# Performance work log

Measured on AMD Instinct MI355X. Metric: run time of the kernel, lower is better.

## Reference

```python
import jax, jax.numpy as jnp
import numpy as np

FEAT_DIM = 128

def conv3(x, w, b):
    y = jax.lax.conv_general_dilated(x, w, (1, 1), 'SAME', dimension_numbers=('NCHW', 'OIHW', 'NCHW'))
    return y + b[None, :, None, None]

def edsr(x, hw, hb, rw, rb, tw, tb):
    # EDSR baseline encoder (no upsampling): head conv, n resblocks, tail conv, global skip
    x = conv3(x, hw, hb)
    res = x
    for i in range(rw.shape[0]):
        t = jax.nn.relu(conv3(res, rw[i, 0], rb[i, 0]))
        res = res + conv3(t, rw[i, 1], rb[i, 1])
    return conv3(res, tw, tb) + x

def maxpool(x, k):
    return jax.lax.reduce_window(x, -jnp.inf, jax.lax.max, (1, 1, k, k), (1, 1, k, k), 'VALID')

def make_coord(h, w):
    ys = -1.0 + (2.0 * jnp.arange(h, dtype=jnp.float32) + 1.0) / h
    xs = -1.0 + (2.0 * jnp.arange(w, dtype=jnp.float32) + 1.0) / w
    yy, xx = jnp.meshgrid(ys, xs, indexing='ij')
    return jnp.stack([yy, xx], axis=-1)  # [h,w,2] (y,x)

def sample_nearest(img, coord):
    # F.grid_sample nearest, align_corners=False, zeros padding.
    # img [b,c,hi,wi]; coord [b,N,2] normalized (y,x) -> [b,N,c]
    b, c, hi, wi = img.shape
    iy = jnp.round(((coord[..., 0] + 1.0) * hi - 1.0) / 2.0)
    ix = jnp.round(((coord[..., 1] + 1.0) * wi - 1.0) / 2.0)
    valid = (iy >= 0) & (iy < hi) & (ix >= 0) & (ix < wi)
    idx = (jnp.clip(iy, 0, hi - 1) * wi + jnp.clip(ix, 0, wi - 1)).astype(jnp.int32)
    out = jnp.take_along_axis(img.reshape(b, c, hi * wi), idx[:, None, :], axis=2)
    out = jnp.where(valid[:, None, :], out, jnp.zeros((), img.dtype))
    return out.transpose(0, 2, 1)

def mlp2(x, w1, b1, w2, b2):
    return jax.nn.gelu(x @ w1 + b1, approximate=False) @ w2 + b2

def level(feat, coord, hr_guide, hr_guide_lr, im_w, im_b, wg, ffn, residual):
    b, c, h, w = feat.shape
    Hh, Ww = hr_guide.shape[2], hr_guide.shape[3]
    N = coord.shape[0]
    coord = jnp.broadcast_to(coord[None], (b, N, 2))
    fc = jnp.broadcast_to(make_coord(h, w).transpose(2, 0, 1)[None], (b, 2, h, w))
    g_s = sample_nearest(hr_guide, coord)  # [b,N,guide_dim]
    scale = jnp.array([h, w], dtype=jnp.float32)
    preds = []
    for vx in (-1.0, 1.0):
        for vy in (-1.0, 1.0):
            coord_ = coord + jnp.array([vx / h, vy / w], dtype=jnp.float32)
            f_s = sample_nearest(feat, coord_)
            gl_s = sample_nearest(hr_guide_lr, coord_)
            c_s = sample_nearest(fc, coord_)
            rel = (coord - c_s) * scale
            inp = jnp.concatenate([f_s, g_s, gl_s, rel], axis=-1)  # [b,N,3*fd+2]
            pred = jax.nn.relu(inp @ im_w + im_b)  # MLP(hidden_list=None): Linear+ReLU
            preds.append(pred[..., :FEAT_DIM])
            preds.append(pred[..., FEAT_DIM:])
    preds = jnp.stack(preds, axis=-2)  # [b,N,8,fd]
    weight = jax.nn.softmax(mlp2(preds, *wg), axis=-2)
    recon = jnp.sum(preds * weight, axis=-2)  # [b,N,fd]
    out = mlp2(recon, *ffn)
    if residual:
        out = out + recon
    return out.transpose(0, 2, 1).reshape(b, -1, Hh, Ww)

def setup_inputs():
    ks = jax.random.split(jax.random.key(0), 24)
    fd, nb, nsb = 128, 31, 3
    B, H, W, hlr = 16, 64, 64, 16
    def w_(k, shape, fan):
        return jax.random.normal(k, shape, dtype=jnp.float32) * (fan ** -0.5)
    return {
        'HR_MSI': jax.random.normal(ks[0], (B, nsb, H, W), dtype=jnp.float32),
        'lms': jax.random.normal(ks[1], (B, nb, H, W), dtype=jnp.float32),
        'LR_HSI': jax.random.normal(ks[2], (B, nb, hlr, hlr), dtype=jnp.float32),
        'spa_head_w': w_(ks[3], (fd, nsb + nb, 3, 3), (nsb + nb) * 9), 'spa_head_b': jnp.zeros((fd,)),
        'spa_res_w': w_(ks[4], (4, 2, fd, fd, 3, 3), fd * 9), 'spa_res_b': jnp.zeros((4, 2, fd)),
        'spa_tail_w': w_(ks[5], (fd, fd, 3, 3), fd * 9), 'spa_tail_b': jnp.zeros((fd,)),
        'spe_head_w': w_(ks[6], (fd, nb, 3, 3), nb * 9), 'spe_head_b': jnp.zeros((fd,)),
        'spe_res_w': w_(ks[7], (4, 2, fd, fd, 3, 3), fd * 9), 'spe_res_b': jnp.zeros((4, 2, fd)),
        'spe_tail_w': w_(ks[8], (fd, fd, 3, 3), fd * 9), 'spe_tail_b': jnp.zeros((fd,)),
        'l1_w': w_(ks[9], (fd * 3 + 2, fd * 2), fd * 3 + 2), 'l1_b': jnp.zeros((fd * 2,)),
        'wg32_w1': w_(ks[10], (fd, 64), fd), 'wg32_b1': jnp.zeros((64,)),
        'wg32_w2': w_(ks[11], (64, fd), 64), 'wg32_b2': jnp.zeros((fd,)),
        'ffn32_w1': w_(ks[12], (fd, 64), fd), 'ffn32_b1': jnp.zeros((64,)),
        'ffn32_w2': w_(ks[13], (64, fd), 64), 'ffn32_b2': jnp.zeros((fd,)),
        'l2_w': w_(ks[14], (fd * 3 + 2, fd * 2), fd * 3 + 2), 'l2_b': jnp.zeros((fd * 2,)),
        'wg64_w1': w_(ks[15], (fd, 64), fd), 'wg64_b1': jnp.zeros((64,)),
        'wg64_w2': w_(ks[16], (64, fd), 64), 'wg64_b2': jnp.zeros((fd,)),
        'ffn64_w1': w_(ks[17], (fd, 64), fd), 'ffn64_b1': jnp.zeros((64,)),
        'ffn64_w2': w_(ks[18], (64, nb), 64), 'ffn64_b2': jnp.zeros((nb,)),
    }

def reference(HR_MSI, lms, LR_HSI, spa_head_w, spa_head_b, spa_res_w, spa_res_b, spa_tail_w, spa_tail_b, spe_head_w, spe_head_b, spe_res_w, spe_res_b, spe_tail_w, spe_tail_b, l1_w, l1_b, wg32_w1, wg32_b1, wg32_w2, wg32_b2, ffn32_w1, ffn32_b1, ffn32_w2, ffn32_b2, l2_w, l2_b, wg64_w1, wg64_b1, wg64_w2, wg64_b2, ffn64_w1, ffn64_b1, ffn64_w2, ffn64_b2):
    b, _, H, W = HR_MSI.shape
    hr_spa = edsr(jnp.concatenate([HR_MSI, lms], axis=1), spa_head_w, spa_head_b, spa_res_w, spa_res_b, spa_tail_w, spa_tail_b)
    guide32 = maxpool(hr_spa, H // 32)   # AdaptiveMaxPool2d -> 32x32
    guide16 = maxpool(hr_spa, H // 16)   # AdaptiveMaxPool2d -> 16x16
    lr_spe = edsr(LR_HSI, spe_head_w, spe_head_b, spe_res_w, spe_res_b, spe_tail_w, spe_tail_b)
    coord32 = make_coord(H // 2, W // 2).reshape(-1, 2)
    coord64 = make_coord(H, W).reshape(-1, 2)
    l1 = level(lr_spe, coord32, guide32, guide16, l1_w, l1_b, (wg32_w1, wg32_b1, wg32_w2, wg32_b2), (ffn32_w1, ffn32_b1, ffn32_w2, ffn32_b2), True)
    l2 = level(l1, coord64, hr_spa, guide32, l2_w, l2_b, (wg64_w1, wg64_b1, wg64_w2, wg64_b2), (ffn64_w1, ffn64_b1, ffn64_w2, ffn64_b2), False)
    return lms + l2
```

## Files before the change

kernel.cpp:

```cpp
#include <hip/hip_runtime.h>
#include <math.h>

typedef _Float16 f16;
typedef __attribute__((ext_vector_type(4))) _Float16 f16x4;
typedef __attribute__((ext_vector_type(8))) _Float16 f16x8;
typedef __attribute__((ext_vector_type(4))) float f32x4;
typedef __attribute__((ext_vector_type(4))) unsigned int u32x4;

__device__ __forceinline__ float gelu_f(float x) {
    float xs = x * 0.70710678118654752440f;
    float ax = fabsf(xs);
    float t = __builtin_amdgcn_rcpf(1.0f + 0.3275911f * ax);
    float p = t * (0.254829592f + t * (-0.284496736f + t * (1.421413741f +
              t * (-1.453152027f + t * 1.061405429f))));
    float erfv = 1.0f - p * __expf(-ax * ax);
    erfv = copysignf(erfv, xs);
    return 0.5f * x * (1.0f + erfv);
}

__device__ __forceinline__ void nsamp(float cy, float cx, int hi, int wi,
                                      int& iy, int& ix, bool& valid) {
    float fy = rintf(((cy + 1.0f) * (float)hi - 1.0f) * 0.5f);
    float fx = rintf(((cx + 1.0f) * (float)wi - 1.0f) * 0.5f);
    valid = (fy >= 0.0f) && (fy < (float)hi) && (fx >= 0.0f) && (fx < (float)wi);
    iy = (int)fminf(fmaxf(fy, 0.0f), (float)(hi - 1));
    ix = (int)fminf(fmaxf(fx, 0.0f), (float)(wi - 1));
}

__global__ __launch_bounds__(256) void pack_w(
    const float* __restrict__ src, f16* __restrict__ dst,
    int Cin, int NCHUNK, int total) {
    int i = blockIdx.x * 256 + threadIdx.x;
    if (i >= total) return;
    int ci = i & 31;
    int tap = (i >> 5) % 9;
    int q = i / 288;
    int chunk = q % NCHUNK;
    int q2 = q / NCHUNK;
    int cout = q2 & 127;
    int conv = q2 >> 7;
    int cin = chunk * 32 + ci;
    float v = (cin < Cin) ? src[((size_t)(conv * 128 + cout) * Cin + cin) * 9 + tap] : 0.f;
    dst[i] = (f16)v;
}

__global__ __launch_bounds__(256) void pack_lvl(
    const float* __restrict__ src, f16* __restrict__ dst,
    int Ksrc, int N, int NC) {
    int i = blockIdx.x * 256 + threadIdx.x;
    if (i >= N * NC * 32) return;
    int kk = i & 31;
    int c = (i >> 5) % NC;
    int n = i / (32 * NC);
    int k = c * 32 + kk;
    dst[i] = (f16)((k < Ksrc) ? src[(size_t)k * N + n] : 0.f);
}

__global__ __launch_bounds__(256) void build_cc(
    const float* __restrict__ msi, const float* __restrict__ lms,
    f16* __restrict__ out, int total) {
    int i = blockIdx.x * 256 + threadIdx.x;
    if (i >= total) return;
    int ch = i % 34;
    int p = i / 34;
    int x = p & 63, y = (p >> 6) & 63, b = p >> 12;
    float v = (ch < 3) ? msi[(((size_t)(b * 3 + ch) << 6) + y << 6) + x]
                       : lms[(((size_t)(b * 31 + ch - 3) << 6) + y << 6) + x];
    out[((size_t)(b * 66 + y + 1) * 66 + x + 1) * 64 + ch] = v;
}

__global__ __launch_bounds__(256) void build_spe(
    const float* __restrict__ in, f16* __restrict__ out, int total) {
    int i = blockIdx.x * 256 + threadIdx.x;
    if (i >= total) return;
    int ch = i % 31;
    int p = i / 31;
    int x = p & 15, y = (p >> 4) & 15, b = p >> 8;
    out[((size_t)(b * 18 + y + 1) * 18 + x + 1) * 32 + ch] =
        (f16)in[(((size_t)(b * 31 + ch) << 4) + y << 4) + x];
}

template<int PXW, int XSH, int ROWS, int WAVES, int NCHUNK>
__global__ __launch_bounds__(WAVES * 64, 4) void conv_mfma(
    const f16* __restrict__ in_h,
    const f16* __restrict__ wp, const float* __restrict__ bias,
    const f16* __restrict__ skip_h, f16* __restrict__ out_h,
    f16* __restrict__ out2, int mode) {
    constexpr int XW = 1 << XSH;
    constexpr int PH = XW + 2;
    constexpr int NPX = (ROWS + 2) * PXW;
    constexpr int UPP = NCHUNK * 4;
    constexpr int UNITS = NPX * UPP;
    constexpr int NTH = WAVES * 64;
    constexpr int ITER = (UNITS + NTH - 1) / NTH;
    constexpr int WN = WAVES / 2;
    constexpr int NT = 8 / WN;
    constexpr int MT = (ROWS << XSH) >> 5;
    constexpr int PXB = NCHUNK * 64;
    __shared__ char ldsb[NPX * PXB];

    int tid = threadIdx.x;
    constexpr int NYB = XW / ROWS;
    int b = blockIdx.x / NYB;
    int y0 = (blockIdx.x % NYB) * ROWS;
    int wave = tid >> 6, lane = tid & 63;
    int wm = wave / WN, wn = wave % WN;
    int l15 = lane & 15, lk = lane >> 4;

#pragma unroll
    for (int i = 0; i < ITER; ++i) {
        int u = tid + NTH * i;
        if (u < UNITS) {
            int px = u / UPP, kg = u % UPP;
            int r = px / PXW, xp = px - r * PXW;
            u32x4 v = *(const u32x4*)(in_h +
                (size_t)((b * PH + y0 + r) * PXW + xp) * (NCHUNK * 32) + kg * 8);
            *(u32x4*)(ldsb + ((u * 16) ^ ((px & 7) << 4))) = v;
        }
    }
    __syncthreads();

    f32x4 acc[MT][NT];
#pragma unroll
    for (int mt = 0; mt < MT; ++mt)
#pragma unroll
        for (int nt = 0; nt < NT; ++nt)
            acc[mt][nt] = (f32x4){0.f, 0.f, 0.f, 0.f};

#pragma unroll
    for (int c = 0; c < NCHUNK; ++c) {
#pragma unroll
        for (int tap = 0; tap < 9; ++tap) {
            const int dy = tap / 3, dx = tap % 3;
            f16x8 afr[MT];
#pragma unroll
            for (int mt = 0; mt < MT; ++mt) {
                int px = (wm * MT + mt) * 16 + l15;
                int row = px >> XSH, x = px & (XW - 1);
                int pxl = (row + dy) * PXW + x + dx;
                int la = pxl * PXB + c * 64 + lk * 16;
                afr[mt] = *(const f16x8*)(ldsb + (la ^ ((pxl & 7) << 4)));
            }
#pragma unroll
            for (int nt = 0; nt < NT; ++nt) {
                int cout = wn * (NT * 16) + nt * 16 + l15;
                f16x8 bfr = *(const f16x8*)(wp + ((size_t)(cout * NCHUNK + c) * 9 + tap) * 32 + lk * 8);
#pragma unroll
                for (int mt = 0; mt < MT; ++mt)
                    acc[mt][nt] = __builtin_amdgcn_mfma_f32_16x16x32_f16(afr[mt], bfr, acc[mt][nt], 0, 0, 0);
            }
        }
    }

#pragma unroll
    for (int mt = 0; mt < MT; ++mt)
#pragma unroll
        for (int nt = 0; nt < NT; ++nt) {
            int cout = wn * (NT * 16) + nt * 16 + l15;
            float bv = bias[cout];
#pragma unroll
            for (int reg = 0; reg < 4; ++reg) {
                int px = (wm * MT + mt) * 16 + lk * 4 + reg;
                int row = px >> XSH, x = px & (XW - 1);
                int yim = y0 + row;
                float vv = acc[mt][nt][reg] + bv;
                size_t ah = ((size_t)(b * PH + yim + 1) * PXW + x + 1) * 128 + cout;
                if (mode == 1) vv = fmaxf(vv, 0.f);
                if (mode == 2) vv += (float)out_h[ah];
                if (mode == 3) {
                    vv += (float)skip_h[ah];
                    out2[((size_t)((b << XSH) + yim) << XSH | x) * 128 + cout] = (f16)vv;
                } else if (mode == 4) {
                    f16 hv = (f16)vv;
                    out_h[ah] = hv;
                    out2[ah] = hv;
                } else {
                    out_h[ah] = (f16)vv;
                }
            }
        }
}

__global__ __launch_bounds__(256) void maxpool_nhwc(
    const f16* __restrict__ in, f16* __restrict__ out,
    int H, int W, int k, int total) {
    int i = blockIdx.x * 256 + threadIdx.x;
    if (i >= total) return;
    int c = i & 127;
    int r = i >> 7;
    int Wo = W / k, Ho = H / k;
    int x = r % Wo; r /= Wo;
    int y = r % Ho;
    int b = r / Ho;
    float m = -3.402823466e38f;
    for (int dy = 0; dy < k; ++dy)
        for (int dx = 0; dx < k; ++dx)
            m = fmaxf(m, (float)in[((size_t)(b * H + y * k + dy) * W + x * k + dx) * 128 + c]);
    out[i] = (f16)m;
}

__global__ __launch_bounds__(256) void level_kernel(
    const f16* __restrict__ featT, int fh, int fw,
    const f16* __restrict__ guideT, int Hg, int Wg,
    const f16* __restrict__ glrT, int hl, int wl,
    int Hq, int Wq, int n_per_b,
    const f16* __restrict__ imw_h, const float* __restrict__ imb,
    const f16* __restrict__ w1h, const float* __restrict__ b1,
    const f16* __restrict__ w2h, const float* __restrict__ b2,
    const f16* __restrict__ f1h, const float* __restrict__ fb1,
    const f16* __restrict__ f2h, const float* __restrict__ fb2,
    int odim, int residual, int out_nchw,
    const float* __restrict__ lms,
    f16* __restrict__ out16, float* __restrict__ outf) {
    __shared__ char smem[58624];
    f16* s_inp  = (f16*)smem;
    f16* s_pred = (f16*)smem;
    f16* s_h1   = (f16*)(smem + 34816);
    f16* s_hh   = (f16*)smem;
    f16* s_rec  = (f16*)(smem + 54272);

    int tid = threadIdx.x;
    int b = blockIdx.x / n_per_b;
    int n0 = (blockIdx.x % n_per_b) * 16;
    float invHq = 1.0f / (float)Hq, invWq = 1.0f / (float)Wq;
    float invfh = 1.0f / (float)fh, invfw = 1.0f / (float)fw;
    int wave = tid >> 6, lane = tid & 63;
    int l15 = lane & 15, lk = lane >> 4;

    {
        const int r64 = tid >> 2, t4 = tid & 3;
        const int cidx = r64 >> 4, q = r64 & 15;
        int n = n0 + q;
        int qy = n / Wq, qx = n - qy * Wq;
        float cy = -1.0f + (float)(2 * qy + 1) * invHq;
        float cx = -1.0f + (float)(2 * qx + 1) * invWq;
        float vxc = (cidx < 2) ? -1.0f : 1.0f;
        float vyc = (cidx & 1) ? 1.0f : -1.0f;
        float cy_ = cy + vxc * invfh;
        float cx_ = cx + vyc * invfw;
        int iy, ix; bool vf;
        nsamp(cy_, cx_, fh, fw, iy, ix, vf);
        const f16* fp = featT + ((size_t)(b * fh + iy) * fw + ix) * 128;
        int gy, gx; bool vg0;
        nsamp(cy, cx, Hg, Wg, gy, gx, vg0);
        const f16* gp = guideT + ((size_t)(b * Hg + gy) * Wg + gx) * 128;
        int ly, lx; bool vl;
        nsamp(cy_, cx_, hl, wl, ly, lx, vl);
        const f16* lp = glrT + ((size_t)(b * hl + ly) * wl + lx) * 128;
        f16* row = s_inp + r64 * 424;
        const u32x4 zz = (u32x4){0, 0, 0, 0};
#pragma unroll
        for (int e = 0; e < 4; ++e) {
            int d0 = t4 * 8 + e * 32;
            u32x4 av = vf ? *(const u32x4*)(fp + d0) : zz;
            u32x4 gv = vg0 ? *(const u32x4*)(gp + d0) : zz;
            u32x4 lv = vl ? *(const u32x4*)(lp + d0) : zz;
            *(u32x4*)(row + d0) = av;
            *(u32x4*)(row + 128 + d0) = gv;
            *(u32x4*)(row + 256 + d0) = lv;
        }
        if (t4 == 0) {
#pragma unroll
            for (int e = 0; e < 4; ++e)
                *(u32x4*)((char*)row + 768 + e * 16) = zz;
            float csy = vf ? (-1.0f + (float)(2 * iy + 1) * invfh) : 0.0f;
            float csx = vf ? (-1.0f + (float)(2 * ix + 1) * invfw) : 0.0f;
            row[384] = (f16)((cy - csy) * (float)fh);
            row[385] = (f16)((cx - csx) * (float)fw);
        }
    }
    __syncthreads();

    f32x4 acc[4][4];
    {
#pragma unroll
        for (int mt = 0; mt < 4; ++mt)
#pragma unroll
            for (int nt = 0; nt < 4; ++nt)
                acc[mt][nt] = (f32x4){0.f, 0.f, 0.f, 0.f};
        int nbase = wave * 64;
#pragma unroll
        for (int ks = 0; ks < 13; ++ks) {
            f16x8 afr[4];
#pragma unroll
            for (int mt = 0; mt < 4; ++mt)
                afr[mt] = *(const f16x8*)((char*)s_inp + (mt * 16 + l15) * 848 + ks * 64 + lk * 16);
#pragma unroll
            for (int nt = 0; nt < 4; ++nt) {
                f16x8 bfr = *(const f16x8*)(imw_h + ((size_t)(nbase + nt * 16 + l15) * 13 + ks) * 32 + lk * 8);
#pragma unroll
                for (int mt = 0; mt < 4; ++mt)
                    acc[mt][nt] = __builtin_amdgcn_mfma_f32_16x16x32_f16(afr[mt], bfr, acc[mt][nt], 0, 0, 0);
            }
        }
    }
    __syncthreads();

    {
        int nbase = wave * 64;
#pragma unroll
        for (int nt = 0; nt < 4; ++nt) {
            int col = nbase + nt * 16 + l15;
            float bv = imb[col];
            int j_hi = col >> 7, d = col & 127;
#pragma unroll
            for (int mt = 0; mt < 4; ++mt)
#pragma unroll
                for (int reg = 0; reg < 4; ++reg) {
                    int row64 = mt * 16 + lk * 4 + reg;
                    int q = row64 & 15, cidx = row64 >> 4;
                    int qj = q * 8 + cidx * 2 + j_hi;
                    s_pred[qj * 136 + d] = (f16)fmaxf(acc[mt][nt][reg] + bv, 0.f);
                }
        }
    }
    __syncthreads();

    {
        f32x4 a1[8];
#pragma unroll
        for (int mt = 0; mt < 8; ++mt) a1[mt] = (f32x4){0.f, 0.f, 0.f, 0.f};
        int c1 = wave * 16 + l15;
#pragma unroll
        for (int ks = 0; ks < 4; ++ks) {
            f16x8 bfr = *(const f16x8*)(w1h + ((size_t)c1 * 4 + ks) * 32 + lk * 8);
#pragma unroll
            for (int mt = 0; mt < 8; ++mt) {
                f16x8 afr = *(const f16x8*)((char*)s_pred + (mt * 16 + l15) * 272 + ks * 64 + lk * 16);
                a1[mt] = __builtin_amdgcn_mfma_f32_16x16x32_f16(afr, bfr, a1[mt], 0, 0, 0);
            }
        }
        float bb1 = b1[c1];
#pragma unroll
        for (int mt = 0; mt < 8; ++mt)
#pragma unroll
            for (int reg = 0; reg < 4; ++reg) {
                int row = mt * 16 + lk * 4 + reg;
                s_h1[row * 72 + c1] = (f16)gelu_f(a1[mt][reg] + bb1);
            }
    }
    __syncthreads();

    {
        f32x4 a2[8][2];
#pragma unroll
        for (int mt = 0; mt < 8; ++mt) {
            a2[mt][0] = (f32x4){0.f, 0.f, 0.f, 0.f};
            a2[mt][1] = (f32x4){0.f, 0.f, 0.f, 0.f};
        }
#pragma unroll
        for (int ks = 0; ks < 2; ++ks) {
#pragma unroll
            for (int nt = 0; nt < 2; ++nt) {
                int c2 = wave * 32 + nt * 16 + l15;
                f16x8 bfr = *(const f16x8*)(w2h + ((size_t)c2 * 2 + ks) * 32 + lk * 8);
#pragma unroll
                for (int mt = 0; mt < 8; ++mt) {
                    f16x8 afr = *(const f16x8*)((char*)s_h1 + (mt * 16 + l15) * 144 + ks * 64 + lk * 16);
                    a2[mt][nt] = __builtin_amdgcn_mfma_f32_16x16x32_f16(afr, bfr, a2[mt][nt], 0, 0, 0);
                }
            }
        }
        int qhalf = lk >> 1;
#pragma unroll
        for (int nt = 0; nt < 2; ++nt) {
            int col = wave * 32 + nt * 16 + l15;
            float bb2 = b2[col];
#pragma unroll
            for (int mt = 0; mt < 8; ++mt) {
                int q = mt * 2 + qhalf;
                float v[4];
                float mloc = -3.4e38f;
#pragma unroll
                for (int reg = 0; reg < 4; ++reg) {
                    v[reg] = a2[mt][nt][reg] + bb2;
                    mloc = fmaxf(mloc, v[reg]);
                }
                float mf = fmaxf(mloc, __shfl_xor(mloc, 16));
                float e[4], sl = 0.f;
#pragma unroll
                for (int reg = 0; reg < 4; ++reg) {
                    e[reg] = __expf(v[reg] - mf);
                    sl += e[reg];
                }
                float sf = sl + __shfl_xor(sl, 16);
                float inv = 1.0f / sf;
                float rp = 0.f;
#pragma unroll
                for (int reg = 0; reg < 4; ++reg) {
                    int row = mt * 16 + lk * 4 + reg;
                    rp += (float)s_pred[row * 136 + col] * e[reg];
                }
                rp *= inv;
                float rf = rp + __shfl_xor(rp, 16);
                if ((lk & 1) == 0) s_rec[q * 136 + col] = (f16)rf;
            }
        }
    }
    __syncthreads();

    {
        f32x4 a1 = (f32x4){0.f, 0.f, 0.f, 0.f};
        int c1 = wave * 16 + l15;
#pragma unroll
        for (int ks = 0; ks < 4; ++ks) {
            f16x8 afr = *(const f16x8*)((char*)s_rec + l15 * 272 + ks * 64 + lk * 16);
            f16x8 bfr = *(const f16x8*)(f1h + ((size_t)c1 * 4 + ks) * 32 + lk * 8);
            a1 = __builtin_amdgcn_mfma_f32_16x16x32_f16(afr, bfr, a1, 0, 0, 0);
        }
        float bb = fb1[c1];
#pragma unroll
        for (int reg = 0; reg < 4; ++reg) {
            int row = lk * 4 + reg;
            s_hh[row * 72 + c1] = (f16)gelu_f(a1[reg] + bb);
        }
    }
    __syncthreads();

    if (!out_nchw) {
        f32x4 a2[2];
        a2[0] = (f32x4){0.f, 0.f, 0.f, 0.f};
        a2[1] = (f32x4){0.f, 0.f, 0.f, 0.f};
#pragma unroll
        for (int ks = 0; ks < 2; ++ks) {
            f16x8 afr = *(const f16x8*)((char*)s_hh + l15 * 144 + ks * 64 + lk * 16);
#pragma unroll
            for (int nt = 0; nt < 2; ++nt) {
                int col = wave * 32 + nt * 16 + l15;
                f16x8 bfr = *(const f16x8*)(f2h + ((size_t)col * 2 + ks) * 32 + lk * 8);
                a2[nt] = __builtin_amdgcn_mfma_f32_16x16x32_f16(afr, bfr, a2[nt], 0, 0, 0);
            }
        }
#pragma unroll
        for (int nt = 0; nt < 2; ++nt) {
            int col = wave * 32 + nt * 16 + l15;
            float bb = fb2[col];
#pragma unroll
            for (int reg = 0; reg < 4; ++reg) {
                int q = lk * 4 + reg;
                int n = n0 + q;
                int qy = n / Wq, qx = n - qy * Wq;
                float val = a2[nt][reg] + bb;
                if (residual) val += (float)s_rec[q * 136 + col];
                out16[((size_t)(b * Hq + qy) * Wq + qx) * 128 + col] = (f16)val;
            }
        }
    } else {
        if (wave < 2) {
            f32x4 a2 = (f32x4){0.f, 0.f, 0.f, 0.f};
#pragma unroll
            for (int ks = 0; ks < 2; ++ks) {
                f16x8 afr = *(const f16x8*)((char*)s_hh + l15 * 144 + ks * 64 + lk * 16);
                int col = wave * 16 + l15;
                f16x8 bfr = *(const f16x8*)(f2h + ((size_t)col * 2 + ks) * 32 + lk * 8);
                a2 = __builtin_amdgcn_mfma_f32_16x16x32_f16(afr, bfr, a2, 0, 0, 0);
            }
            int d = wave * 16 + l15;
            if (d < odim) {
                float bb = fb2[d];
#pragma unroll
                for (int reg = 0; reg < 4; ++reg) {
                    int q = lk * 4 + reg;
                    int n = n0 + q;
                    int qy = n / Wq, qx = n - qy * Wq;
                    size_t oi = (((size_t)b * odim + d) * Hq + qy) * Wq + qx;
                    outf[oi] = a2[reg] + bb + lms[oi];
                }
            }
        }
    }
}

#define WPACK_B   0ull
#define CC_B      5529600ull
#define SPEIN_B   (CC_B)
#define X2_B      (CC_B + 331776ull)
#define R2_B      (CC_B + 1658880ull)
#define T2_B      (CC_B + 2985984ull)
#define RH_B      14450688ull
#define TH_B      32292864ull
#define XH_B      50135040ull
#define G32_B     (TH_B)
#define G16_B     (TH_B + 4194304ull)
#define L1T_B     (TH_B + 5242880ull)
#define LRSPE_B   (CC_B + 4313088ull)
#define HR16_B    67977216ull
#define LVLW_B    101531648ull
#define L1IMW_B   (LVLW_B)
#define L1W1_B    (LVLW_B + 212992ull)
#define L1W2_B    (LVLW_B + 229376ull)
#define L1F1_B    (LVLW_B + 245760ull)
#define L1F2_B    (LVLW_B + 262144ull)
#define L2IMW_B   (LVLW_B + 278528ull)
#define L2W1_B    (LVLW_B + 491520ull)
#define L2W2_B    (LVLW_B + 507904ull)
#define L2F1_B    (LVLW_B + 524288ull)
#define L2F2_B    (LVLW_B + 540672ull)

extern "C" void kernel_launch(void* const* d_in, const int* in_sizes, int n_in,
                              void* d_out, int out_size, void* d_ws, size_t ws_size,
                              hipStream_t stream) {
    (void)in_sizes; (void)n_in; (void)out_size; (void)ws_size;
    const float* HR_MSI     = (const float*)d_in[0];
    const float* lms        = (const float*)d_in[1];
    const float* LR_HSI     = (const float*)d_in[2];
    const float* spa_head_w = (const float*)d_in[3];
    const float* spa_head_b = (const float*)d_in[4];
    const float* spa_res_w  = (const float*)d_in[5];
    const float* spa_res_b  = (const float*)d_in[6];
    const float* spa_tail_w = (const float*)d_in[7];
    const float* spa_tail_b = (const float*)d_in[8];
    const float* spe_head_w = (const float*)d_in[9];
    const float* spe_head_b = (const float*)d_in[10];
    const float* spe_res_w  = (const float*)d_in[11];
    const float* spe_res_b  = (const float*)d_in[12];
    const float* spe_tail_w = (const float*)d_in[13];
    const float* spe_tail_b = (const float*)d_in[14];
    const float* l1_w   = (const float*)d_in[15];
    const float* l1_b   = (const float*)d_in[16];
    const float* wg32_w1 = (const float*)d_in[17];
    const float* wg32_b1 = (const float*)d_in[18];
    const float* wg32_w2 = (const float*)d_in[19];
    const float* wg32_b2 = (const float*)d_in[20];
    const float* ffn32_w1 = (const float*)d_in[21];
    const float* ffn32_b1 = (const float*)d_in[22];
    const float* ffn32_w2 = (const float*)d_in[23];
    const float* ffn32_b2 = (const float*)d_in[24];
    const float* l2_w   = (const float*)d_in[25];
    const float* l2_b   = (const float*)d_in[26];
    const float* wg64_w1 = (const float*)d_in[27];
    const float* wg64_b1 = (const float*)d_in[28];
    const float* wg64_w2 = (const float*)d_in[29];
    const float* wg64_b2 = (const float*)d_in[30];
    const float* ffn64_w1 = (const float*)d_in[31];
    const float* ffn64_b1 = (const float*)d_in[32];
    const float* ffn64_w2 = (const float*)d_in[33];
    const float* ffn64_b2 = (const float*)d_in[34];

    char* ws = (char*)d_ws;
    f16* Wp      = (f16*)(ws + WPACK_B);
    f16* Cc      = (f16*)(ws + CC_B);
    f16* SPEin   = (f16*)(ws + SPEIN_B);
    f16* X2h     = (f16*)(ws + X2_B);
    f16* R2h     = (f16*)(ws + R2_B);
    f16* T2h     = (f16*)(ws + T2_B);
    f16* lrspe16 = (f16*)(ws + LRSPE_B);
    f16* Rh      = (f16*)(ws + RH_B);
    f16* Xh      = (f16*)(ws + XH_B);
    f16* Th      = (f16*)(ws + TH_B);
    f16* g32T    = (f16*)(ws + G32_B);
    f16* g16T    = (f16*)(ws + G16_B);
    f16* l1T16   = (f16*)(ws + L1T_B);
    f16* hr16    = (f16*)(ws + HR16_B);
    f16* l1imw = (f16*)(ws + L1IMW_B);
    f16* l1w1  = (f16*)(ws + L1W1_B);
    f16* l1w2  = (f16*)(ws + L1W2_B);
    f16* l1f1  = (f16*)(ws + L1F1_B);
    f16* l1f2  = (f16*)(ws + L1F2_B);
    f16* l2imw = (f16*)(ws + L2IMW_B);
    f16* l2w1  = (f16*)(ws + L2W1_B);
    f16* l2w2  = (f16*)(ws + L2W2_B);
    f16* l2f1  = (f16*)(ws + L2F1_B);
    f16* l2f2  = (f16*)(ws + L2F2_B);

    hipMemsetAsync(ws + CC_B, 0, 8921088ull, stream);
    hipMemsetAsync(ws + RH_B, 0, 53526528ull, stream);

    pack_w<<<288, 256, 0, stream>>>(spa_head_w, Wp + 0, 34, 2, 73728);
    pack_w<<<4608, 256, 0, stream>>>(spa_res_w, Wp + 73728, 128, 4, 1179648);
    pack_w<<<576, 256, 0, stream>>>(spa_tail_w, Wp + 1253376, 128, 4, 147456);
    pack_w<<<144, 256, 0, stream>>>(spe_head_w, Wp + 1400832, 31, 1, 36864);
    pack_w<<<4608, 256, 0, stream>>>(spe_res_w, Wp + 1437696, 128, 4, 1179648);
    pack_w<<<576, 256, 0, stream>>>(spe_tail_w, Wp + 2617344, 128, 4, 147456);

    pack_lvl<<<416, 256, 0, stream>>>(l1_w, l1imw, 386, 256, 13);
    pack_lvl<<<32, 256, 0, stream>>>(wg32_w1, l1w1, 128, 64, 4);
    pack_lvl<<<32, 256, 0, stream>>>(wg32_w2, l1w2, 64, 128, 2);
    pack_lvl<<<32, 256, 0, stream>>>(ffn32_w1, l1f1, 128, 64, 4);
    pack_lvl<<<32, 256, 0, stream>>>(ffn32_w2, l1f2, 64, 128, 2);
    pack_lvl<<<416, 256, 0, stream>>>(l2_w, l2imw, 386, 256, 13);
    pack_lvl<<<32, 256, 0, stream>>>(wg64_w1, l2w1, 128, 64, 4);
    pack_lvl<<<32, 256, 0, stream>>>(wg64_w2, l2w2, 64, 128, 2);
    pack_lvl<<<32, 256, 0, stream>>>(ffn64_w1, l2f1, 128, 64, 4);
    pack_lvl<<<8, 256, 0, stream>>>(ffn64_w2, l2f2, 64, 31, 2);

    build_cc<<<8704, 256, 0, stream>>>(HR_MSI, lms, Cc, 16 * 64 * 64 * 34);
    conv_mfma<66, 6, 2, 8, 2><<<512, 512, 0, stream>>>(Cc, Wp + 0, spa_head_b,
                                                       nullptr, Xh, Rh, 4);
    hipMemsetAsync(ws + SPEIN_B, 0, 5361664ull, stream);
    for (int i = 0; i < 4; ++i) {
        conv_mfma<66, 6, 2, 8, 4><<<512, 512, 0, stream>>>(
            Rh, Wp + 73728 + (size_t)(2 * i) * 147456, spa_res_b + 2 * i * 128,
            nullptr, Th, nullptr, 1);
        conv_mfma<66, 6, 2, 8, 4><<<512, 512, 0, stream>>>(
            Th, Wp + 73728 + (size_t)(2 * i + 1) * 147456, spa_res_b + (2 * i + 1) * 128,
            nullptr, Rh, nullptr, 2);
    }
    conv_mfma<66, 6, 2, 8, 4><<<512, 512, 0, stream>>>(Rh, Wp + 1253376, spa_tail_b,
                                                       Xh, nullptr, hr16, 3);

    maxpool_nhwc<<<8192, 256, 0, stream>>>(hr16, g32T, 64, 64, 2, 2097152);
    maxpool_nhwc<<<2048, 256, 0, stream>>>(hr16, g16T, 64, 64, 4, 524288);

    build_spe<<<496, 256, 0, stream>>>(LR_HSI, SPEin, 16 * 16 * 16 * 31);
    conv_mfma<18, 4, 2, 4, 1><<<128, 256, 0, stream>>>(SPEin, Wp + 1400832, spe_head_b,
                                                       nullptr, X2h, R2h, 4);
    for (int i = 0; i < 4; ++i) {
        conv_mfma<18, 4, 2, 4, 4><<<128, 256, 0, stream>>>(
            R2h, Wp + 1437696 + (size_t)(2 * i) * 147456, spe_res_b + 2 * i * 128,
            nullptr, T2h, nullptr, 1);
        conv_mfma<18, 4, 2, 4, 4><<<128, 256, 0, stream>>>(
            T2h, Wp + 1437696 + (size_t)(2 * i + 1) * 147456, spe_res_b + (2 * i + 1) * 128,
            nullptr, R2h, nullptr, 2);
    }
    conv_mfma<18, 4, 2, 4, 4><<<128, 256, 0, stream>>>(R2h, Wp + 2617344, spe_tail_b,
                                                       X2h, nullptr, lrspe16, 3);

    level_kernel<<<1024, 256, 0, stream>>>(
        lrspe16, 16, 16, g32T, 32, 32, g16T, 16, 16,
        32, 32, 64,
        l1imw, l1_b, l1w1, wg32_b1, l1w2, wg32_b2,
        l1f1, ffn32_b1, l1f2, ffn32_b2,
        128, 1, 0, nullptr, l1T16, nullptr);

    level_kernel<<<4096, 256, 0, stream>>>(
        l1T16, 32, 32, hr16, 64, 64, g32T, 32, 32,
        64, 64, 256,
        l2imw, l2_b, l2w1, wg64_b1, l2w2, wg64_b2,
        l2f1, ffn64_b1, l2f2, ffn64_b2,
        31, 0, 1, lms, nullptr, (float*)d_out);
}
```

Before: 1.027 ms.

## Co-schedule spatial and spectral EDSR convs in shared launches, merge maxpools

Adds a dual-conv kernel that dispatches blocks to either the high-resolution spatial EDSR conv or the low-resolution spectral EDSR conv based on block index. The two independent encoders now run in the same launches, so the small spectral convs fill the machine alongside the large ones instead of running serially. The spectral buffers get their own workspace region so they no longer alias buffers still in use, and the two maxpools become one launch. The spectral path now runs with 8 waves instead of 4, which may change its tiling efficiency.

Measured after the change: 941.7 us. 1.09x faster.

```diff
diff --git a/kernel.cpp b/kernel.cpp
--- a/kernel.cpp
+++ b/kernel.cpp
@@ -81,7 +81,8 @@
 }
 
 template<int PXW, int XSH, int ROWS, int WAVES, int NCHUNK>
-__global__ __launch_bounds__(WAVES * 64, 4) void conv_mfma(
+__device__ __forceinline__ void conv_body(
+    int bx, char* ldsb,
     const f16* __restrict__ in_h,
     const f16* __restrict__ wp, const float* __restrict__ bias,
     const f16* __restrict__ skip_h, f16* __restrict__ out_h,
@@ -97,12 +98,11 @@
     constexpr int NT = 8 / WN;
     constexpr int MT = (ROWS << XSH) >> 5;
     constexpr int PXB = NCHUNK * 64;
-    __shared__ char ldsb[NPX * PXB];
 
     int tid = threadIdx.x;
     constexpr int NYB = XW / ROWS;
-    int b = blockIdx.x / NYB;
-    int y0 = (blockIdx.x % NYB) * ROWS;
+    int b = bx / NYB;
+    int y0 = (bx % NYB) * ROWS;
     int wave = tid >> 6, lane = tid & 63;
     int wm = wave / WN, wn = wave % WN;
     int l15 = lane & 15, lk = lane >> 4;
@@ -181,22 +181,57 @@
         }
 }
 
-__global__ __launch_bounds__(256) void maxpool_nhwc(
-    const f16* __restrict__ in, f16* __restrict__ out,
-    int H, int W, int k, int total) {
+template<int PXW1, int XSH1, int ROWS1, int NCH1,
+         int PXW2, int XSH2, int ROWS2, int NCH2, int WAVES>
+__global__ __launch_bounds__(WAVES * 64, 4) void conv_dual(
+    int g1,
+    const f16* __restrict__ in1, const f16* __restrict__ wp1,
+    const float* __restrict__ bi1, const f16* __restrict__ sk1,
+    f16* __restrict__ o1h, f16* __restrict__ o1b,
+    const f16* __restrict__ in2, const f16* __restrict__ wp2,
+    const float* __restrict__ bi2, const f16* __restrict__ sk2,
+    f16* __restrict__ o2h, f16* __restrict__ o2b,
+    int mode) {
+    constexpr int B1 = (ROWS1 + 2) * PXW1 * NCH1 * 64;
+    constexpr int B2 = (ROWS2 + 2) * PXW2 * NCH2 * 64;
+    constexpr int MAXB = B1 > B2 ? B1 : B2;
+    __shared__ char ldsb[MAXB];
+    int bx = blockIdx.x;
+    if (bx < g1)
+        conv_body<PXW1, XSH1, ROWS1, WAVES, NCH1>(bx, ldsb, in1, wp1, bi1, sk1, o1h, o1b, mode);
+    else
+        conv_body<PXW2, XSH2, ROWS2, WAVES, NCH2>(bx - g1, ldsb, in2, wp2, bi2, sk2, o2h, o2b, mode);
+}
+
+__global__ __launch_bounds__(256) void maxpool_both(
+    const f16* __restrict__ in, f16* __restrict__ o2, f16* __restrict__ o4) {
     int i = blockIdx.x * 256 + threadIdx.x;
-    if (i >= total) return;
-    int c = i & 127;
-    int r = i >> 7;
-    int Wo = W / k, Ho = H / k;
-    int x = r % Wo; r /= Wo;
-    int y = r % Ho;
-    int b = r / Ho;
-    float m = -3.402823466e38f;
-    for (int dy = 0; dy < k; ++dy)
-        for (int dx = 0; dx < k; ++dx)
-            m = fmaxf(m, (float)in[((size_t)(b * H + y * k + dy) * W + x * k + dx) * 128 + c]);
-    out[i] = (f16)m;
+    if (i < 2097152) {
+        int c = i & 127;
+        int r = i >> 7;
+        int x = r & 31; r >>= 5;
+        int y = r & 31; r >>= 5;
+        int b = r;
+        float m = -3.402823466e38f;
+        for (int dy = 0; dy < 2; ++dy)
+            for (int dx = 0; dx < 2; ++dx)
+                m = fmaxf(m, (float)in[((size_t)((b * 64 + y * 2 + dy)) * 64 + x * 2 + dx) * 128 + c]);
+        o2[i] = (f16)m;
+    } else {
+        int j = i - 2097152;
+        if (j < 524288) {
+            int c = j & 127;
+            int r = j >> 7;
+            int x = r & 15; r >>= 4;
+            int y = r & 15; r >>= 4;
+            int b = r;
+            float m = -3.402823466e38f;
+            for (int dy = 0; dy < 4; ++dy)
+                for (int dx = 0; dx < 4; ++dx)
+                    m = fmaxf(m, (float)in[((size_t)((b * 64 + y * 4 + dy)) * 64 + x * 4 + dx) * 128 + c]);
+            o4[j] = (f16)m;
+        }
+    }
 }
 
 __global__ __launch_bounds__(256) void level_kernel(
@@ -473,17 +508,12 @@
 
 #define WPACK_B   0ull
 #define CC_B      5529600ull
-#define SPEIN_B   (CC_B)
-#define X2_B      (CC_B + 331776ull)
-#define R2_B      (CC_B + 1658880ull)
-#define T2_B      (CC_B + 2985984ull)
 #define RH_B      14450688ull
 #define TH_B      32292864ull
 #define XH_B      50135040ull
 #define G32_B     (TH_B)
 #define G16_B     (TH_B + 4194304ull)
 #define L1T_B     (TH_B + 5242880ull)
-#define LRSPE_B   (CC_B + 4313088ull)
 #define HR16_B    67977216ull
 #define LVLW_B    101531648ull
 #define L1IMW_B   (LVLW_B)
@@ -496,6 +526,12 @@
 #define L2W2_B    (LVLW_B + 507904ull)
 #define L2F1_B    (LVLW_B + 524288ull)
 #define L2F2_B    (LVLW_B + 540672ull)
+#define SPE2_B    102088704ull
+#define SPEIN_B   (SPE2_B)
+#define X2_B      (SPE2_B + 331776ull)
+#define R2_B      (SPE2_B + 1658880ull)
+#define T2_B      (SPE2_B + 2985984ull)
+#define LRSPE_B   (SPE2_B + 4313088ull)
 
 extern "C" void kernel_launch(void* const* d_in, const int* in_sizes, int n_in,
                               void* d_out, int out_size, void* d_ws, size_t ws_size,
@@ -565,6 +601,7 @@
 
     hipMemsetAsync(ws + CC_B, 0, 8921088ull, stream);
     hipMemsetAsync(ws + RH_B, 0, 53526528ull, stream);
+    hipMemsetAsync(ws + SPE2_B, 0, 5361664ull, stream);
 
     pack_w<<<288, 256, 0, stream>>>(spa_head_w, Wp + 0, 34, 2, 73728);
     pack_w<<<4608, 256, 0, stream>>>(spa_res_w, Wp + 73728, 128, 4, 1179648);
@@ -585,36 +622,28 @@
     pack_lvl<<<8, 256, 0, stream>>>(ffn64_w2, l2f2, 64, 31, 2);
 
     build_cc<<<8704, 256, 0, stream>>>(HR_MSI, lms, Cc, 16 * 64 * 64 * 34);
-    conv_mfma<66, 6, 2, 8, 2><<<512, 512, 0, stream>>>(Cc, Wp + 0, spa_head_b,
-                                                       nullptr, Xh, Rh, 4);
-    hipMemsetAsync(ws + SPEIN_B, 0, 5361664ull, stream);
+    build_spe<<<496, 256, 0, stream>>>(LR_HSI, SPEin, 16 * 16 * 16 * 31);
+
+    conv_dual<66, 6, 2, 2, 18, 4, 2, 1, 8><<<640, 512, 0, stream>>>(
+        512,
+        Cc, Wp + 0, spa_head_b, nullptr, Xh, Rh,
+        SPEin, Wp + 1400832, spe_head_b, nullptr, X2h, R2h, 4);
     for (int i = 0; i < 4; ++i) {
-        conv_mfma<66, 6, 2, 8, 4><<<512, 512, 0, stream>>>(
-            Rh, Wp + 73728 + (size_t)(2 * i) * 147456, spa_res_b + 2 * i * 128,
-            nullptr, Th, nullptr, 1);
-        conv_mfma<66, 6, 2, 8, 4><<<512, 512, 0, stream>>>(
-            Th, Wp + 73728 + (size_t)(2 * i + 1) * 147456, spa_res_b + (2 * i + 1) * 128,
-            nullptr, Rh, nullptr, 2);
-    }
-    conv_mfma<66, 6, 2, 8, 4><<<512, 512, 0, stream>>>(Rh, Wp + 1253376, spa_tail_b,
-                                                       Xh, nullptr, hr16, 3);
-
-    maxpool_nhwc<<<8192, 256, 0, stream>>>(hr16, g32T, 64, 64, 2, 2097152);
-    maxpool_nhwc<<<2048, 256, 0, stream>>>(hr16, g16T, 64, 64, 4, 524288);
-
-    build_spe<<<496, 256, 0, stream>>>(LR_HSI, SPEin, 16 * 16 * 16 * 31);
-    conv_mfma<18, 4, 2, 4, 1><<<128, 256, 0, stream>>>(SPEin, Wp + 1400832, spe_head_b,
-                                                       nullptr, X2h, R2h, 4);
-    for (int i = 0; i < 4; ++i) {
-        conv_mfma<18, 4, 2, 4, 4><<<128, 256, 0, stream>>>(
-            R2h, Wp + 1437696 + (size_t)(2 * i) * 147456, spe_res_b + 2 * i * 128,
-            nullptr, T2h, nullptr, 1);
-        conv_mfma<18, 4, 2, 4, 4><<<128, 256, 0, stream>>>(
-            T2h, Wp + 1437696 + (size_t)(2 * i + 1) * 147456, spe_res_b + (2 * i + 1) * 128,
-            nullptr, R2h, nullptr, 2);
-    }
-    conv_mfma<18, 4, 2, 4, 4><<<128, 256, 0, stream>>>(R2h, Wp + 2617344, spe_tail_b,
-                                                       X2h, nullptr, lrspe16, 3);
+        conv_dual<66, 6, 2, 4, 18, 4, 2, 4, 8><<<640, 512, 0, stream>>>(
+            512,
+            Rh, Wp + 73728 + (size_t)(2 * i) * 147456, spa_res_b + 2 * i * 128, nullptr, Th, nullptr,
+            R2h, Wp + 1437696 + (size_t)(2 * i) * 147456, spe_res_b + 2 * i * 128, nullptr, T2h, nullptr, 1);
+        conv_dual<66, 6, 2, 4, 18, 4, 2, 4, 8><<<640, 512, 0, stream>>>(
+            512,
+            Th, Wp + 73728 + (size_t)(2 * i + 1) * 147456, spa_res_b + (2 * i + 1) * 128, nullptr, Rh, nullptr,
+            T2h, Wp + 1437696 + (size_t)(2 * i + 1) * 147456, spe_res_b + (2 * i + 1) * 128, nullptr, R2h, nullptr, 2);
+    }
+    conv_dual<66, 6, 2, 4, 18, 4, 2, 4, 8><<<640, 512, 0, stream>>>(
+        512,
+        Rh, Wp + 1253376, spa_tail_b, Xh, nullptr, hr16,
+        R2h, Wp + 2617344, spe_tail_b, X2h, nullptr, lrspe16, 3);
+
+    maxpool_both<<<10240, 256, 0, stream>>>(hr16, g32T, g16T);
 
     level_kernel<<<1024, 256, 0, stream>>>(
         lrspe16, 16, 16, g32T, 32, 32, g16T, 16, 16,
```
